# Kernel tuning notes

Hardware: AMD Instinct MI355X
Metric: run time of the kernel (lower is better)

The kernel has to match this reference:

```python
import jax, jax.numpy as jnp
import numpy as np

NUM_CAMS = 4
E = 256          # embed_dim
H_HEADS = 8      # num_heads
DH = E // H_HEADS
CIN = 64
FF = 4 * E
N_LAYERS = 2
EPS = 1e-5


def _layer_norm(x, g, b):
    mu = jnp.mean(x, axis=-1, keepdims=True)
    var = jnp.mean((x - mu) ** 2, axis=-1, keepdims=True)
    return (x - mu) * jax.lax.rsqrt(var + EPS) * g + b


def setup_inputs() -> dict:
    key = jax.random.key(0)
    ks = jax.random.split(key, 20)
    s = 0.02
    inp = {
        "features": jax.random.normal(ks[0], (NUM_CAMS, 2, CIN, 96, 96), jnp.float32),
        # 1x1 input projection conv
        "Wp": jax.random.normal(ks[1], (E, CIN), jnp.float32) * s,
        "bp": jnp.zeros((E,), jnp.float32),
        # per-layer attention params (stacked over 2 layers)
        "Wqkv": jax.random.normal(ks[2], (N_LAYERS, 3 * E, E), jnp.float32) * s,
        "bqkv": jnp.zeros((N_LAYERS, 3 * E), jnp.float32),
        "Wo": jax.random.normal(ks[3], (N_LAYERS, E, E), jnp.float32) * s,
        "bo": jnp.zeros((N_LAYERS, E), jnp.float32),
        # FFN
        "W1": jax.random.normal(ks[4], (N_LAYERS, FF, E), jnp.float32) * s,
        "b1": jnp.zeros((N_LAYERS, FF), jnp.float32),
        "W2": jax.random.normal(ks[5], (N_LAYERS, E, FF), jnp.float32) * s,
        "b2": jnp.zeros((N_LAYERS, E), jnp.float32),
        # LayerNorms
        "g1": jnp.ones((N_LAYERS, E), jnp.float32),
        "be1": jnp.zeros((N_LAYERS, E), jnp.float32),
        "g2": jnp.ones((N_LAYERS, E), jnp.float32),
        "be2": jnp.zeros((N_LAYERS, E), jnp.float32),
        # 1x1 output conv
        "Wout": jax.random.normal(ks[6], (CIN, E), jnp.float32) * s,
        "bout": jnp.zeros((CIN,), jnp.float32),
    }
    return inp


def reference(features, Wp, bp, Wqkv, bqkv, Wo, bo, W1, b1, W2, b2,
              g1, be1, g2, be2, Wout, bout):
    n_cam, B, Cin, Hh, Ww = features.shape
    # 1x1 conv projection + rearrange to per-pixel sequences: [B*H*W, n_cam, E]
    x = jnp.einsum('nbchw,ec->bhwne', features, Wp) + bp
    x = x.reshape(B * Hh * Ww, n_cam, E)

    scale = 1.0 / jnp.sqrt(jnp.float32(DH))
    for i in range(N_LAYERS):
        # self-attention (post-norm encoder layer, dropout=identity in eval)
        qkv = x @ Wqkv[i].T + bqkv[i]                      # [N, S, 3E]
        q, k, v = jnp.split(qkv, 3, axis=-1)
        q = q.reshape(-1, n_cam, H_HEADS, DH)
        k = k.reshape(-1, n_cam, H_HEADS, DH)
        v = v.reshape(-1, n_cam, H_HEADS, DH)
        scores = jnp.einsum('nqhd,nkhd->nhqk', q, k) * scale
        attn = jax.nn.softmax(scores, axis=-1)
        sa = jnp.einsum('nhqk,nkhd->nqhd', attn, v).reshape(-1, n_cam, E)
        sa = sa @ Wo[i].T + bo[i]
        x = _layer_norm(x + sa, g1[i], be1[i])
        # FFN (ReLU activation, default)
        ff = jax.nn.relu(x @ W1[i].T + b1[i]) @ W2[i].T + b2[i]
        x = _layer_norm(x + ff, g2[i], be2[i])

    # mean over cameras, back to [B, C, H, W] via 1x1 output conv
    fused = x.mean(axis=1).reshape(B, Hh, Ww, E)
    out = jnp.einsum('bhwe,ce->bchw', fused, Wout) + bout[None, :, None, None]
    return out
```

## Files before the change

kernel.cpp:

```cpp
#include <hip/hip_runtime.h>
#include <cstdint>
#include <cstddef>


typedef __bf16 bf16;
typedef __bf16 bf16x8 __attribute__((ext_vector_type(8)));
typedef __bf16 bf16x4 __attribute__((ext_vector_type(4)));
typedef float  f32x4  __attribute__((ext_vector_type(4)));

__device__ __forceinline__ void async_copy16(const void* g, void* l)
{
    __builtin_amdgcn_global_load_lds(
        (__attribute__((address_space(1))) void*)g,
        (__attribute__((address_space(3))) void*)l,
        16, 0, 0);
}

#define WAITV8_BAR() asm volatile("s_waitcnt vmcnt(8)\ns_barrier" ::: "memory")
#define WAITV4_BAR() asm volatile("s_waitcnt vmcnt(4)\ns_barrier" ::: "memory")
#define WAITV0_BAR() asm volatile("s_waitcnt vmcnt(0)\ns_barrier" ::: "memory")
#define WAITL_BAR()  asm volatile("s_waitcnt lgkmcnt(0)\ns_barrier" ::: "memory")

__global__ void pack_all_k(const float* __restrict__ s0, const float* __restrict__ s1,
                           const float* __restrict__ s2, const float* __restrict__ s3,
                           const float* __restrict__ s4,
                           bf16* __restrict__ d0, bf16* __restrict__ d1,
                           bf16* __restrict__ d2, bf16* __restrict__ d3,
                           bf16* __restrict__ d4)
{
    const int i = blockIdx.x * 256 + threadIdx.x;
    if (i < 393216)       d0[i] = (bf16)s0[i];
    else if (i < 524288)  d1[i - 393216] = (bf16)s1[i - 393216];
    else if (i < 1048576) {
        const int j = i - 524288;
        const int l = j >> 18, r = j & 262143;
        const int e     = r & 7;
        const int idx16 = r >> 3;
        const int l16   = idx16 & 15;
        const int quad  = (idx16 >> 4) & 3;
        const int nt    = (idx16 >> 6) & 7;
        const int kk    = (idx16 >> 9) & 1;
        const int q     = (idx16 >> 10) & 3;
        const int hc    = idx16 >> 12;
        const int row   = hc * 128 + nt * 16 + l16;
        const int k     = q * 64 + (kk * 4 + quad) * 8 + e;
        d2[j] = (bf16)s2[l * 262144 + row * 256 + k];
    } else if (i < 1572864) {
        const int j = i - 1048576;
        const int l = j >> 18, r = j & 262143;
        const int e     = r & 7;
        const int idx16 = r >> 3;
        const int l16   = idx16 & 15;
        const int quad  = (idx16 >> 4) & 3;
        const int nt    = (idx16 >> 6) & 15;
        const int q     = (idx16 >> 10) & 3;
        const int hc    = idx16 >> 12;
        const int n     = nt * 16 + l16;
        const int k     = hc * 128 + q * 32 + quad * 8 + e;
        d3[j] = (bf16)s3[l * 262144 + n * 1024 + k];
    }
    else                  d4[i - 1572864] = (bf16)s4[i - 1572864];
}

__global__ __launch_bounds__(256) void feat_pack_k(const float* __restrict__ feat,
                                                   bf16* __restrict__ Xf)
{
    __shared__ float ft[64][68];

    const int tid  = threadIdx.x;
    const int camb = blockIdx.y;
    const int cam  = camb >> 1;
    const int b    = camb & 1;
    const int hw0  = blockIdx.x * 64;

    const float* fb = feat + (size_t)camb * 64 * 9216 + hw0;
#pragma unroll
    for (int rep = 0; rep < 16; ++rep) {
        const int idx = rep * 256 + tid;
        const int c = idx >> 6, p = idx & 63;
        ft[p][c] = fb[(size_t)c * 9216 + p];
    }
    __syncthreads();

    const int pbase = b * 9216 + hw0;
#pragma unroll
    for (int rep = 0; rep < 2; ++rep) {
        const int idx = rep * 256 + tid;
        const int p = idx >> 3, cc = idx & 7;
        const f32x4 a = *(const f32x4*)(&ft[p][cc * 8]);
        const f32x4 c4 = *(const f32x4*)(&ft[p][cc * 8 + 4]);
        bf16x8 v;
#pragma unroll
        for (int i = 0; i < 4; ++i) { v[i] = (bf16)a[i]; v[4 + i] = (bf16)c4[i]; }
        const size_t t = (size_t)(pbase + p) * 4 + cam;
        *(bf16x8*)(Xf + t * 64 + cc * 8) = v;
    }
}

template <bool RELU>
__global__ __launch_bounds__(256, 2) void gemm_bt(
    const bf16* __restrict__ A, const bf16* __restrict__ B,
    const float* __restrict__ bias, bf16* __restrict__ C,
    int N, int K)
{
    __shared__ __align__(16) char smem[65536];

    const int tid  = threadIdx.x;
    const int lane = tid & 63;
    const int wv   = tid >> 6;
    const int wm   = wv >> 1;
    const int wn   = wv & 1;
    const int bm   = blockIdx.y * 128;
    const int bn   = blockIdx.x * 128;

    const int r8  = lane >> 3;
    const int p8  = lane & 7;
    const int gch = p8 ^ r8;

    const int quad = lane >> 4;
    const int l16  = lane & 15;

    f32x4 acc[4][4] = {};
    const int nk = K >> 6;

    auto STAGE = [&](int kc, char* base) {
#pragma unroll
        for (int inst = 0; inst < 4; ++inst) {
            const int row = wv * 32 + inst * 8 + r8;
            async_copy16(A + (size_t)(bm + row) * K + (kc * 64 + gch * 8),
                         base + (wv * 4 + inst) * 1024);
            async_copy16(B + (size_t)(bn + row) * K + (kc * 64 + gch * 8),
                         base + 16384 + (wv * 4 + inst) * 1024);
        }
    };

    STAGE(0, smem);

#pragma unroll 1
    for (int kc = 0; kc < nk; ++kc) {
        const char* cur = smem + (size_t)(kc & 1) * 32768;
        if (kc + 1 < nk) {
            STAGE(kc + 1, smem + (size_t)((kc + 1) & 1) * 32768);
            WAITV8_BAR();
        } else {
            WAITV0_BAR();
        }

#pragma unroll
        for (int kk = 0; kk < 2; ++kk) {
            bf16x8 af[4], bfr[4];
            const int lch = kk * 4 + quad;
#pragma unroll
            for (int i = 0; i < 4; ++i) {
                const int m = wm * 64 + i * 16 + l16;
                af[i] = *(const bf16x8*)(cur + (m * 8 + (lch ^ (m & 7))) * 16);
                const int n = wn * 64 + i * 16 + l16;
                bfr[i] = *(const bf16x8*)(cur + 16384 + (n * 8 + (lch ^ (n & 7))) * 16);
            }
            __builtin_amdgcn_s_setprio(1);
#pragma unroll
            for (int i = 0; i < 4; ++i)
#pragma unroll
                for (int j = 0; j < 4; ++j)
                    acc[i][j] = __builtin_amdgcn_mfma_f32_16x16x32_bf16(
                        af[i], bfr[j], acc[i][j], 0, 0, 0);
            __builtin_amdgcn_s_setprio(0);
        }
        WAITL_BAR();
    }

#pragma unroll
    for (int j = 0; j < 4; ++j) {
        const int n = bn + wn * 64 + j * 16 + l16;
        const float bv = bias[n];
#pragma unroll
        for (int i = 0; i < 4; ++i) {
            const int mb = bm + wm * 64 + i * 16 + quad * 4;
#pragma unroll
            for (int r = 0; r < 4; ++r) {
                float v = acc[i][j][r] + bv;
                if (RELU) v = fmaxf(v, 0.f);
                C[(size_t)(mb + r) * N + n] = (bf16)v;
            }
        }
    }
}

__device__ __forceinline__ void wo_stage(const bf16* __restrict__ Wo, int kc,
                                         char* buf, int tid)
{
#pragma unroll
    for (int it = 0; it < 4; ++it) {
        const int L = it * 256 + tid;
        const int r128 = L >> 3, psl = L & 7;
        const int g = psl ^ (r128 & 7);
        const int n = r128 * 2 + (g >> 2);
        const int c = g & 3;
        async_copy16(Wo + (size_t)n * 256 + kc * 32 + c * 8,
                     buf + (size_t)L * 16);
    }
}

__global__ __launch_bounds__(256, 2) void attn_ln_k(
    const bf16* __restrict__ QKV, const bf16* __restrict__ Wo,
    const float* __restrict__ bias, const bf16* __restrict__ Xres,
    const float* __restrict__ gam, const float* __restrict__ bet,
    bf16* __restrict__ Xout)
{
    __shared__ __align__(16) char smem[66560];
    bf16* SAs  = (bf16*)smem;
    char* Bbuf = smem + 32768;
    float2 (*red)[2] = (float2 (*)[2])(void*)(smem + 65536);

    const int tid  = threadIdx.x;
    const int lane = tid & 63;
    const int wv   = tid >> 6;
    const int wm   = wv >> 1;
    const int wn   = wv & 1;
    const int quad = lane >> 4;
    const int l16  = lane & 15;
    const int bm   = blockIdx.x * 64;

    wo_stage(Wo, 0, Bbuf, tid);

    {
        const int hh = lane >> 3;
        const int cg = lane & 7;
        const int s0 = blockIdx.x * 16;
        const float SCALE = 0.17677669529663687f;

#pragma unroll
        for (int g = 0; g < 4; ++g) {
            const int seq = s0 + g * 4 + wv;
            const bf16* bse = QKV + (size_t)seq * 3072 + hh * 32 + cg * 4;

            float qf[4][4], kf[4][4], vf[4][4];
#pragma unroll
            for (int i = 0; i < 4; ++i) {
                const bf16x4 qb = *(const bf16x4*)(bse + i * 768);
                const bf16x4 kb = *(const bf16x4*)(bse + i * 768 + 256);
                const bf16x4 vb = *(const bf16x4*)(bse + i * 768 + 512);
#pragma unroll
                for (int d = 0; d < 4; ++d) {
                    qf[i][d] = (float)qb[d];
                    kf[i][d] = (float)kb[d];
                    vf[i][d] = (float)vb[d];
                }
            }

            float sc[4][4];
#pragma unroll
            for (int i = 0; i < 4; ++i)
#pragma unroll
                for (int j = 0; j < 4; ++j)
                    sc[i][j] = qf[i][0] * kf[j][0] + qf[i][1] * kf[j][1]
                             + qf[i][2] * kf[j][2] + qf[i][3] * kf[j][3];

#pragma unroll
            for (int msk = 1; msk <= 4; msk <<= 1)
#pragma unroll
                for (int i = 0; i < 4; ++i)
#pragma unroll
                    for (int j = 0; j < 4; ++j)
                        sc[i][j] += __shfl_xor(sc[i][j], msk, 64);

#pragma unroll
            for (int i = 0; i < 4; ++i) {
                const float v0 = sc[i][0] * SCALE, v1 = sc[i][1] * SCALE;
                const float v2 = sc[i][2] * SCALE, v3 = sc[i][3] * SCALE;
                const float mx = fmaxf(fmaxf(v0, v1), fmaxf(v2, v3));
                const float e0 = expf(v0 - mx), e1 = expf(v1 - mx);
                const float e2 = expf(v2 - mx), e3 = expf(v3 - mx);
                const float inv = 1.f / (e0 + e1 + e2 + e3);
                sc[i][0] = e0 * inv; sc[i][1] = e1 * inv;
                sc[i][2] = e2 * inv; sc[i][3] = e3 * inv;
            }

#pragma unroll
            for (int i = 0; i < 4; ++i) {
                bf16x4 ov;
#pragma unroll
                for (int d = 0; d < 4; ++d) {
                    const float o = sc[i][0] * vf[0][d] + sc[i][1] * vf[1][d]
                                  + sc[i][2] * vf[2][d] + sc[i][3] * vf[3][d];
                    ov[d] = (bf16)o;
                }
                const int m  = (g * 4 + wv) * 4 + i;
                const int gc = lane >> 1;
                const int sl = (gc & 24) | ((gc ^ m) & 7);
                *(bf16x4*)((char*)SAs + (m * 32 + sl) * 16 + (lane & 1) * 8) = ov;
            }
        }
    }
    __syncthreads();

    f32x4 acc[2][8] = {};

#pragma unroll
    for (int s = 0; s < 8; ++s) {
        const char* cur = Bbuf + (size_t)(s & 1) * 16384;
        if (s < 7) {
            wo_stage(Wo, s + 1, Bbuf + (size_t)((s + 1) & 1) * 16384, tid);
            WAITV4_BAR();
        } else {
            WAITV0_BAR();
        }
        const int gc = s * 4 + quad;
        bf16x8 af[2], bfr[8];
#pragma unroll
        for (int i = 0; i < 2; ++i) {
            const int m  = wm * 32 + i * 16 + l16;
            const int sl = (gc & 24) | ((gc ^ m) & 7);
            af[i] = *(const bf16x8*)((const char*)SAs + (m * 32 + sl) * 16);
        }
#pragma unroll
        for (int j = 0; j < 8; ++j) {
            const int n  = wn * 128 + j * 16 + l16;
            const int sl = (((n & 1) * 4 + quad) ^ ((n >> 1) & 7)) & 7;
            bfr[j] = *(const bf16x8*)(cur + ((n >> 1) * 8 + sl) * 16);
        }
        __builtin_amdgcn_s_setprio(1);
#pragma unroll
        for (int i = 0; i < 2; ++i)
#pragma unroll
            for (int j = 0; j < 8; ++j)
                acc[i][j] = __builtin_amdgcn_mfma_f32_16x16x32_bf16(
                    af[i], bfr[j], acc[i][j], 0, 0, 0);
        __builtin_amdgcn_s_setprio(0);
        WAITL_BAR();
    }

    float bv[8], gv[8], bev[8];
#pragma unroll
    for (int j = 0; j < 8; ++j) {
        const int n = wn * 128 + j * 16 + l16;
        bv[j] = bias[n]; gv[j] = gam[n]; bev[j] = bet[n];
    }

#pragma unroll
    for (int i = 0; i < 2; ++i) {
#pragma unroll
        for (int r = 0; r < 4; ++r) {
            const int rl = wm * 32 + i * 16 + quad * 4 + r;
            const size_t row = (size_t)(bm + rl);
            float s1 = 0.f, s2 = 0.f;
#pragma unroll
            for (int j = 0; j < 8; ++j) {
                const int n = wn * 128 + j * 16 + l16;
                const float v = acc[i][j][r] + bv[j] + (float)Xres[row * 256 + n];
                acc[i][j][r] = v;
                s1 += v; s2 += v * v;
            }
#pragma unroll
            for (int off = 1; off < 16; off <<= 1) {
                s1 += __shfl_xor(s1, off, 64);
                s2 += __shfl_xor(s2, off, 64);
            }
            if (l16 == 0) red[rl][wn] = make_float2(s1, s2);
        }
    }
    __syncthreads();

#pragma unroll
    for (int i = 0; i < 2; ++i) {
#pragma unroll
        for (int r = 0; r < 4; ++r) {
            const int rl = wm * 32 + i * 16 + quad * 4 + r;
            const float2 p0 = red[rl][0], p1 = red[rl][1];
            const float mu  = (p0.x + p1.x) * (1.f / 256.f);
            const float ex2 = (p0.y + p1.y) * (1.f / 256.f);
            const float rstd = rsqrtf(fmaxf(ex2 - mu * mu, 0.f) + 1e-5f);
            const size_t row = (size_t)(bm + rl);
#pragma unroll
            for (int j = 0; j < 8; ++j) {
                const int n = wn * 128 + j * 16 + l16;
                Xout[row * 256 + n] = (bf16)((acc[i][j][r] - mu) * rstd * gv[j] + bev[j]);
            }
        }
    }
}

__global__ __launch_bounds__(256, 3) void ffn_fused_k(
    const bf16* __restrict__ X,
    const bf16* __restrict__ W1P, const float* __restrict__ b1,
    const bf16* __restrict__ W2P, const float* __restrict__ b2,
    const float* __restrict__ gam, const float* __restrict__ bet,
    bf16* __restrict__ Xout)
{
    __shared__ __align__(16) char smem[49152];
    bf16* Xs = (bf16*)smem;
    bf16* Ts = (bf16*)(smem + 32768);
    float2 (*red)[4] = (float2 (*)[4])(void*)(smem + 32768);

    const int tid  = threadIdx.x;
    const int lane = tid & 63;
    const int wn   = tid >> 6;
    const int quad = lane >> 4;
    const int l16  = lane & 15;
    const int bm   = blockIdx.x * 64;
    const int rot  = (blockIdx.x >> 3) & 7;

#pragma unroll
    for (int it = 0; it < 8; ++it) {
        const int L = it * 256 + tid;
        const int row = L >> 5, slot = L & 31;
        const int gch = (slot & 24) | ((slot ^ row) & 7);
        async_copy16(X + (size_t)(bm + row) * 256 + gch * 8,
                     (char*)Xs + (size_t)L * 16);
    }
    WAITV0_BAR();

    f32x4 acc2[4][4] = {};

#pragma unroll 1
    for (int hc = 0; hc < 8; ++hc) {
        const int hcr = (hc + rot) & 7;
        float b1v[2];
#pragma unroll
        for (int j = 0; j < 2; ++j)
            b1v[j] = b1[hcr * 128 + wn * 32 + j * 16 + l16];

        f32x4 accA[4][2] = {};

#pragma unroll
        for (int q = 0; q < 4; ++q) {
#pragma unroll
            for (int kk = 0; kk < 2; ++kk) {
                const int ch = kk * 4 + quad;
                const int gc = q * 8 + ch;
                bf16x8 af[4], bfr[2];
#pragma unroll
                for (int j = 0; j < 2; ++j)
                    bfr[j] = *(const bf16x8*)(W1P +
                        ((size_t)(((hcr * 4 + q) * 2 + kk) * 8) + wn * 2 + j) * 512
                        + lane * 8);
#pragma unroll
                for (int i = 0; i < 4; ++i) {
                    const int m  = i * 16 + l16;
                    const int sl = (gc & 24) | ((gc ^ m) & 7);
                    af[i] = *(const bf16x8*)((const char*)Xs + (m * 32 + sl) * 16);
                }
                __builtin_amdgcn_s_setprio(1);
#pragma unroll
                for (int i = 0; i < 4; ++i)
#pragma unroll
                    for (int j = 0; j < 2; ++j)
                        accA[i][j] = __builtin_amdgcn_mfma_f32_16x16x32_bf16(
                            af[i], bfr[j], accA[i][j], 0, 0, 0);
                __builtin_amdgcn_s_setprio(0);
            }
        }

#pragma unroll
        for (int j = 0; j < 2; ++j) {
            const int h  = wn * 32 + j * 16 + l16;
            const float bb = b1v[j];
            const int g  = h >> 3;
#pragma unroll
            for (int i = 0; i < 4; ++i)
#pragma unroll
                for (int r = 0; r < 4; ++r) {
                    const int m  = i * 16 + quad * 4 + r;
                    const int sl = (g & 8) | ((g ^ m) & 7);
                    const float v = fmaxf(accA[i][j][r] + bb, 0.f);
                    *((bf16*)((char*)Ts + (m * 16 + sl) * 16 + (h & 7) * 2)) = (bf16)v;
                }
        }
        WAITL_BAR();

#pragma unroll
        for (int q = 0; q < 4; ++q) {
            const int tc = q * 4 + quad;
            bf16x8 af[4], bfr[4];
#pragma unroll
            for (int j = 0; j < 4; ++j)
                bfr[j] = *(const bf16x8*)(W2P +
                    ((size_t)((hcr * 4 + q) * 16) + wn * 4 + j) * 512
                    + lane * 8);
#pragma unroll
            for (int i = 0; i < 4; ++i) {
                const int m  = i * 16 + l16;
                const int sl = (tc & 8) | ((tc ^ m) & 7);
                af[i] = *(const bf16x8*)((const char*)Ts + (m * 16 + sl) * 16);
            }
            __builtin_amdgcn_s_setprio(1);
#pragma unroll
            for (int i = 0; i < 4; ++i)
#pragma unroll
                for (int j = 0; j < 4; ++j)
                    acc2[i][j] = __builtin_amdgcn_mfma_f32_16x16x32_bf16(
                        af[i], bfr[j], acc2[i][j], 0, 0, 0);
            __builtin_amdgcn_s_setprio(0);
        }
        WAITL_BAR();
    }

    float bv[4], gv[4], bev[4];
#pragma unroll
    for (int j = 0; j < 4; ++j) {
        const int n = wn * 64 + j * 16 + l16;
        bv[j] = b2[n]; gv[j] = gam[n]; bev[j] = bet[n];
    }

#pragma unroll
    for (int i = 0; i < 4; ++i) {
#pragma unroll
        for (int r = 0; r < 4; ++r) {
            const int rl = i * 16 + quad * 4 + r;
            float s1 = 0.f, s2 = 0.f;
#pragma unroll
            for (int j = 0; j < 4; ++j) {
                const int n  = wn * 64 + j * 16 + l16;
                const int gc = n >> 3;
                const int sl = (gc & 24) | ((gc ^ rl) & 7);
                const float xr = (float)*((const bf16*)((const char*)Xs +
                                   (rl * 32 + sl) * 16 + (n & 7) * 2));
                const float v = acc2[i][j][r] + bv[j] + xr;
                acc2[i][j][r] = v;
                s1 += v; s2 += v * v;
            }
#pragma unroll
            for (int off = 1; off < 16; off <<= 1) {
                s1 += __shfl_xor(s1, off, 64);
                s2 += __shfl_xor(s2, off, 64);
            }
            if (l16 == 0) red[rl][wn] = make_float2(s1, s2);
        }
    }
    __syncthreads();

#pragma unroll
    for (int i = 0; i < 4; ++i) {
#pragma unroll
        for (int r = 0; r < 4; ++r) {
            const int rl = i * 16 + quad * 4 + r;
            const float2 p0 = red[rl][0], p1 = red[rl][1];
            const float2 p2 = red[rl][2], p3 = red[rl][3];
            const float mu  = (p0.x + p1.x + p2.x + p3.x) * (1.f / 256.f);
            const float ex2 = (p0.y + p1.y + p2.y + p3.y) * (1.f / 256.f);
            const float rstd = rsqrtf(fmaxf(ex2 - mu * mu, 0.f) + 1e-5f);
            const size_t row = (size_t)(bm + rl);
#pragma unroll
            for (int j = 0; j < 4; ++j) {
                const int n = wn * 64 + j * 16 + l16;
                Xout[row * 256 + n] = (bf16)((acc2[i][j][r] - mu) * rstd * gv[j] + bev[j]);
            }
        }
    }
}

__global__ __launch_bounds__(256) void out_proj_k(const bf16* __restrict__ X,
                                                  const float* __restrict__ Wout,
                                                  const float* __restrict__ bout,
                                                  float* __restrict__ out)
{
    __shared__ float fused[16][260];
    const int tid = threadIdx.x;
    const int p0  = blockIdx.x * 16;

#pragma unroll
    for (int it = 0; it < 16; ++it) {
        const int idx = it * 256 + tid;
        const int pix = idx >> 8, e = idx & 255;
        const size_t base = (size_t)(p0 + pix) * 1024 + e;
        const float s = (float)X[base] + (float)X[base + 256] +
                        (float)X[base + 512] + (float)X[base + 768];
        fused[pix][e] = s * 0.25f;
    }
    __syncthreads();

    const int pix = tid & 15;
    const int c0  = tid >> 4;
    const int p   = p0 + pix;
    const int b   = p / 9216;
    const int hw  = p % 9216;
#pragma unroll
    for (int it = 0; it < 4; ++it) {
        const int c = it * 16 + c0;
        const float* w = Wout + c * 256;
        float acc = bout[c];
#pragma unroll 8
        for (int e = 0; e < 256; ++e) acc += fused[pix][e] * w[e];
        out[((size_t)b * 64 + c) * 9216 + hw] = acc;
    }
}

extern "C" void kernel_launch(void* const* d_in, const int* in_sizes, int n_in,
                              void* d_out, int out_size, void* d_ws, size_t ws_size,
                              hipStream_t stream)
{
    const float* features = (const float*)d_in[0];
    const float* Wp   = (const float*)d_in[1];
    const float* bp   = (const float*)d_in[2];
    const float* Wqkv = (const float*)d_in[3];
    const float* bqkv = (const float*)d_in[4];
    const float* Wo   = (const float*)d_in[5];
    const float* bo   = (const float*)d_in[6];
    const float* W1   = (const float*)d_in[7];
    const float* b1   = (const float*)d_in[8];
    const float* W2   = (const float*)d_in[9];
    const float* b2   = (const float*)d_in[10];
    const float* g1   = (const float*)d_in[11];
    const float* be1  = (const float*)d_in[12];
    const float* g2   = (const float*)d_in[13];
    const float* be2  = (const float*)d_in[14];
    const float* Wout = (const float*)d_in[15];
    const float* bout = (const float*)d_in[16];
    float* out = (float*)d_out;

    char* ws = (char*)d_ws;
    bf16* X   = (bf16*)(ws);
    bf16* QKV = (bf16*)(ws + 37748736ull);
    bf16* Xf  = (bf16*)(ws + 188743680ull);
    bf16* WpB = (bf16*)(ws + 198180864ull);
    bf16* Wb  = (bf16*)(ws + 226492416ull);

    bf16* WqkvB = Wb;
    bf16* WoB   = Wb + 393216;
    bf16* W1B   = Wb + 524288;
    bf16* W2B   = Wb + 1048576;

    pack_all_k<<<6208, 256, 0, stream>>>(Wqkv, Wo, W1, W2, Wp,
                                         WqkvB, WoB, W1B, W2B, WpB);

    feat_pack_k<<<dim3(144, 8), 256, 0, stream>>>(features, Xf);
    gemm_bt<false><<<dim3(2, 576), 256, 0, stream>>>(Xf, WpB, bp, X, 256, 64);

    for (int l = 0; l < 2; ++l) {
        gemm_bt<false><<<dim3(6, 576), 256, 0, stream>>>(
            X, WqkvB + l * 196608, bqkv + l * 768, QKV, 768, 256);
        attn_ln_k<<<1152, 256, 0, stream>>>(
            QKV, WoB + l * 65536, bo + l * 256, X,
            g1 + l * 256, be1 + l * 256, X);
        ffn_fused_k<<<1152, 256, 0, stream>>>(
            X, W1B + l * 262144, b1 + l * 1024,
            W2B + l * 262144, b2 + l * 256,
            g2 + l * 256, be2 + l * 256, X);
    }

    out_proj_k<<<1152, 256, 0, stream>>>(X, Wout, bout, out);
}
```

Measured before the change: 569.6 us.

## Pre-pack QKV and Wo weights into MFMA fragment layout and read directly

Repacks Wqkv and Wo during the weight pack kernel into per-lane MFMA fragment order. A new QKV GEMM kernel stages only A tiles in LDS and reads B fragments straight from global/L2. attn_ln_k drops its LDS double-buffered Wo staging and per-step barriers, with 4 waves each owning 64 output columns. It also rotates the k-order per block to spread L2 traffic. The aim is to cut LDS use and barriers, allowing 3 blocks per CU, at the cost of more global and L2 reads for weights.

```diff
diff --git a/kernel.cpp b/kernel.cpp
--- a/kernel.cpp
+++ b/kernel.cpp
@@ -29,9 +29,36 @@
                            bf16* __restrict__ d4)
 {
     const int i = blockIdx.x * 256 + threadIdx.x;
-    if (i < 393216)       d0[i] = (bf16)s0[i];
-    else if (i < 524288)  d1[i - 393216] = (bf16)s1[i - 393216];
-    else if (i < 1048576) {
+    if (i < 393216) {
+        const int j = i;
+        const int l = (j >= 196608) ? 1 : 0;
+        const int r = j - l * 196608;
+        const int e     = r & 7;
+        const int idx16 = r >> 3;
+        const int lane  = idx16 & 63;
+        const int l16   = lane & 15;
+        const int quad  = lane >> 4;
+        const int frag  = idx16 >> 6;
+        const int ckk   = frag / 48;
+        const int nt    = frag - ckk * 48;
+        const int kc    = ckk >> 1, kk = ckk & 1;
+        const int n     = nt * 16 + l16;
+        const int k     = kc * 64 + (kk * 4 + quad) * 8 + e;
+        d0[j] = (bf16)s0[l * 196608 + n * 256 + k];
+    } else if (i < 524288) {
+        const int j = i - 393216;
+        const int l = j >> 16, r = j & 65535;
+        const int e     = r & 7;
+        const int idx16 = r >> 3;
+        const int lane  = idx16 & 63;
+        const int l16   = lane & 15;
+        const int quad  = lane >> 4;
+        const int frag  = idx16 >> 6;
+        const int s     = frag >> 4, nt = frag & 15;
+        const int n     = nt * 16 + l16;
+        const int k     = s * 32 + quad * 8 + e;
+        d1[j] = (bf16)s1[l * 65536 + n * 256 + k];
+    } else if (i < 1048576) {
         const int j = i - 524288;
         const int l = j >> 18, r = j & 262143;
         const int e     = r & 7;
@@ -186,42 +213,107 @@
     }
 }
 
-__device__ __forceinline__ void wo_stage(const bf16* __restrict__ Wo, int kc,
-                                         char* buf, int tid)
-{
-#pragma unroll
-    for (int it = 0; it < 4; ++it) {
-        const int L = it * 256 + tid;
-        const int r128 = L >> 3, psl = L & 7;
-        const int g = psl ^ (r128 & 7);
-        const int n = r128 * 2 + (g >> 2);
-        const int c = g & 3;
-        async_copy16(Wo + (size_t)n * 256 + kc * 32 + c * 8,
-                     buf + (size_t)L * 16);
-    }
-}
-
-__global__ __launch_bounds__(256, 2) void attn_ln_k(
-    const bf16* __restrict__ QKV, const bf16* __restrict__ Wo,
+__global__ __launch_bounds__(256, 3) void gemm_qkv_k(
+    const bf16* __restrict__ A, const bf16* __restrict__ BP,
+    const float* __restrict__ bias, bf16* __restrict__ C)
+{
+    __shared__ __align__(16) char smem[32768];
+
+    const int tid  = threadIdx.x;
+    const int lane = tid & 63;
+    const int wv   = tid >> 6;
+    const int wn   = wv;
+    const int bm   = blockIdx.y * 128;
+    const int bn   = blockIdx.x * 128;
+    const int ntb  = blockIdx.x * 8;
+
+    const int r8  = lane >> 3;
+    const int p8  = lane & 7;
+    const int gch = p8 ^ r8;
+    const int quad = lane >> 4;
+    const int l16  = lane & 15;
+
+    f32x4 acc[8][2] = {};
+
+    auto STAGE = [&](int kc, char* base) {
+#pragma unroll
+        for (int inst = 0; inst < 4; ++inst) {
+            const int row = wv * 32 + inst * 8 + r8;
+            async_copy16(A + (size_t)(bm + row) * 256 + (kc * 64 + gch * 8),
+                         base + (wv * 4 + inst) * 1024);
+        }
+    };
+
+    STAGE(0, smem);
+
+#pragma unroll
+    for (int kc = 0; kc < 4; ++kc) {
+        const char* cur = smem + (size_t)(kc & 1) * 16384;
+        if (kc < 3) {
+            STAGE(kc + 1, smem + (size_t)((kc + 1) & 1) * 16384);
+            WAITV4_BAR();
+        } else {
+            WAITV0_BAR();
+        }
+
+#pragma unroll
+        for (int kk = 0; kk < 2; ++kk) {
+            const int lch = kk * 4 + quad;
+            bf16x8 af[8], bfr[2];
+#pragma unroll
+            for (int j = 0; j < 2; ++j)
+                bfr[j] = *(const bf16x8*)(BP +
+                    ((size_t)((kc * 2 + kk) * 48 + ntb + wn * 2 + j)) * 512
+                    + lane * 8);
+#pragma unroll
+            for (int i = 0; i < 8; ++i) {
+                const int m = i * 16 + l16;
+                af[i] = *(const bf16x8*)(cur + (m * 8 + (lch ^ (m & 7))) * 16);
+            }
+            __builtin_amdgcn_s_setprio(1);
+#pragma unroll
+            for (int i = 0; i < 8; ++i)
+#pragma unroll
+                for (int j = 0; j < 2; ++j)
+                    acc[i][j] = __builtin_amdgcn_mfma_f32_16x16x32_bf16(
+                        af[i], bfr[j], acc[i][j], 0, 0, 0);
+            __builtin_amdgcn_s_setprio(0);
+        }
+        WAITL_BAR();
+    }
+
+#pragma unroll
+    for (int j = 0; j < 2; ++j) {
+        const int n = bn + wn * 32 + j * 16 + l16;
+        const float bv = bias[n];
+#pragma unroll
+        for (int i = 0; i < 8; ++i) {
+            const int mb = bm + i * 16 + quad * 4;
+#pragma unroll
+            for (int r = 0; r < 4; ++r)
+                C[(size_t)(mb + r) * 768 + n] = (bf16)(acc[i][j][r] + bv);
+        }
+    }
+}
+
+__global__ __launch_bounds__(256, 3) void attn_ln_k(
+    const bf16* __restrict__ QKV, const bf16* __restrict__ WoP,
     const float* __restrict__ bias, const bf16* __restrict__ Xres,
     const float* __restrict__ gam, const float* __restrict__ bet,
     bf16* __restrict__ Xout)
 {
-    __shared__ __align__(16) char smem[66560];
-    bf16* SAs  = (bf16*)smem;
-    char* Bbuf = smem + 32768;
-    float2 (*red)[2] = (float2 (*)[2])(void*)(smem + 65536);
+    __shared__ __align__(16) char smem[34816];
+    bf16* SAs = (bf16*)smem;
+    float2 (*red)[4] = (float2 (*)[4])(void*)(smem + 32768);
 
     const int tid  = threadIdx.x;
     const int lane = tid & 63;
     const int wv   = tid >> 6;
-    const int wm   = wv >> 1;
-    const int wn   = wv & 1;
+    const int wn   = wv;
     const int quad = lane >> 4;
     const int l16  = lane & 15;
     const int bm   = blockIdx.x * 64;
-
-    wo_stage(Wo, 0, Bbuf, tid);
+    const int rot  = (blockIdx.x >> 3) & 7;
 
     {
         const int hh = lane >> 3;
@@ -294,59 +386,50 @@
     }
     __syncthreads();
 
-    f32x4 acc[2][8] = {};
+    f32x4 acc[4][4] = {};
 
 #pragma unroll
     for (int s = 0; s < 8; ++s) {
-        const char* cur = Bbuf + (size_t)(s & 1) * 16384;
-        if (s < 7) {
-            wo_stage(Wo, s + 1, Bbuf + (size_t)((s + 1) & 1) * 16384, tid);
-            WAITV4_BAR();
-        } else {
-            WAITV0_BAR();
-        }
-        const int gc = s * 4 + quad;
-        bf16x8 af[2], bfr[8];
-#pragma unroll
-        for (int i = 0; i < 2; ++i) {
-            const int m  = wm * 32 + i * 16 + l16;
+        const int sr = (s + rot) & 7;
+        const int gc = sr * 4 + quad;
+        bf16x8 af[4], bfr[4];
+#pragma unroll
+        for (int j = 0; j < 4; ++j)
+            bfr[j] = *(const bf16x8*)(WoP +
+                ((size_t)(sr * 16 + wn * 4 + j)) * 512 + lane * 8);
+#pragma unroll
+        for (int i = 0; i < 4; ++i) {
+            const int m  = i * 16 + l16;
             const int sl = (gc & 24) | ((gc ^ m) & 7);
             af[i] = *(const bf16x8*)((const char*)SAs + (m * 32 + sl) * 16);
         }
-#pragma unroll
-        for (int j = 0; j < 8; ++j) {
-            const int n  = wn * 128 + j * 16 + l16;
-            const int sl = (((n & 1) * 4 + quad) ^ ((n >> 1) & 7)) & 7;
-            bfr[j] = *(const bf16x8*)(cur + ((n >> 1) * 8 + sl) * 16);
-        }
         __builtin_amdgcn_s_setprio(1);
 #pragma unroll
-        for (int i = 0; i < 2; ++i)
-#pragma unroll
-            for (int j = 0; j < 8; ++j)
+        for (int i = 0; i < 4; ++i)
+#pragma unroll
+            for (int j = 0; j < 4; ++j)
                 acc[i][j] = __builtin_amdgcn_mfma_f32_16x16x32_bf16(
                     af[i], bfr[j], acc[i][j], 0, 0, 0);
         __builtin_amdgcn_s_setprio(0);
-        WAITL_BAR();
-    }
-
-    float bv[8], gv[8], bev[8];
-#pragma unroll
-    for (int j = 0; j < 8; ++j) {
-        const int n = wn * 128 + j * 16 + l16;
+    }
+
+    float bv[4], gv[4], bev[4];
+#pragma unroll
+    for (int j = 0; j < 4; ++j) {
+        const int n = wn * 64 + j * 16 + l16;
         bv[j] = bias[n]; gv[j] = gam[n]; bev[j] = bet[n];
     }
 
 #pragma unroll
-    for (int i = 0; i < 2; ++i) {
+    for (int i = 0; i < 4; ++i) {
 #pragma unroll
         for (int r = 0; r < 4; ++r) {
-            const int rl = wm * 32 + i * 16 + quad * 4 + r;
+            const int rl = i * 16 + quad * 4 + r;
             const size_t row = (size_t)(bm + rl);
             float s1 = 0.f, s2 = 0.f;
 #pragma unroll
-            for (int j = 0; j < 8; ++j) {
-                const int n = wn * 128 + j * 16 + l16;
+            for (int j = 0; j < 4; ++j) {
+                const int n = wn * 64 + j * 16 + l16;
                 const float v = acc[i][j][r] + bv[j] + (float)Xres[row * 256 + n];
                 acc[i][j][r] = v;
                 s1 += v; s2 += v * v;
@@ -362,18 +445,19 @@
     __syncthreads();
 
 #pragma unroll
-    for (int i = 0; i < 2; ++i) {
+    for (int i = 0; i < 4; ++i) {
 #pragma unroll
         for (int r = 0; r < 4; ++r) {
-            const int rl = wm * 32 + i * 16 + quad * 4 + r;
+            const int rl = i * 16 + quad * 4 + r;
             const float2 p0 = red[rl][0], p1 = red[rl][1];
-            const float mu  = (p0.x + p1.x) * (1.f / 256.f);
-            const float ex2 = (p0.y + p1.y) * (1.f / 256.f);
+            const float2 p2 = red[rl][2], p3 = red[rl][3];
+            const float mu  = (p0.x + p1.x + p2.x + p3.x) * (1.f / 256.f);
+            const float ex2 = (p0.y + p1.y + p2.y + p3.y) * (1.f / 256.f);
             const float rstd = rsqrtf(fmaxf(ex2 - mu * mu, 0.f) + 1e-5f);
             const size_t row = (size_t)(bm + rl);
 #pragma unroll
-            for (int j = 0; j < 8; ++j) {
-                const int n = wn * 128 + j * 16 + l16;
+            for (int j = 0; j < 4; ++j) {
+                const int n = wn * 64 + j * 16 + l16;
                 Xout[row * 256 + n] = (bf16)((acc[i][j][r] - mu) * rstd * gv[j] + bev[j]);
             }
         }
@@ -399,6 +483,7 @@
     const int l16  = lane & 15;
     const int bm   = blockIdx.x * 64;
     const int rot  = (blockIdx.x >> 3) & 7;
+    const int rot2 = (blockIdx.x >> 6) & 3;
 
 #pragma unroll
     for (int it = 0; it < 8; ++it) {
@@ -423,7 +508,8 @@
         f32x4 accA[4][2] = {};
 
 #pragma unroll
-        for (int q = 0; q < 4; ++q) {
+        for (int q0 = 0; q0 < 4; ++q0) {
+            const int q = (q0 + rot2) & 3;
 #pragma unroll
             for (int kk = 0; kk < 2; ++kk) {
                 const int ch = kk * 4 + quad;
@@ -469,7 +555,8 @@
         WAITL_BAR();
 
 #pragma unroll
-        for (int q = 0; q < 4; ++q) {
+        for (int q0 = 0; q0 < 4; ++q0) {
+            const int q = (q0 + rot2) & 3;
             const int tc = q * 4 + quad;
             bf16x8 af[4], bfr[4];
 #pragma unroll
@@ -627,8 +714,8 @@
     gemm_bt<false><<<dim3(2, 576), 256, 0, stream>>>(Xf, WpB, bp, X, 256, 64);
 
     for (int l = 0; l < 2; ++l) {
-        gemm_bt<false><<<dim3(6, 576), 256, 0, stream>>>(
-            X, WqkvB + l * 196608, bqkv + l * 768, QKV, 768, 256);
+        gemm_qkv_k<<<dim3(6, 576), 256, 0, stream>>>(
+            X, WqkvB + l * 196608, bqkv + l * 768, QKV);
         attn_ln_k<<<1152, 256, 0, stream>>>(
             QKV, WoB + l * 65536, bo + l * 256, X,
             g1 + l * 256, be1 + l * 256, X);
```

New measurement: 572.0 us. About the same (+0.4%).
